# Kernel optimization log

Hardware: AMD Instinct MI355X
Metric: run time of the kernel (lower is better)

Reference implementation:

```python
import jax, jax.numpy as jnp
import numpy as np

B, L, D, H = 2, 2048, 1024, 16
HD = D // H
HID = 4 * D
EPS = 1e-5


def setup_inputs() -> dict:
    key = jax.random.key(0)
    ks = jax.random.split(key, 16)
    s = 0.02
    inp = {
        "x": jax.random.normal(ks[0], (B, L, D), jnp.float32),
        "mask": jnp.triu(jnp.ones((L, L), bool), k=1),  # True above diagonal -> masked
        "wq": jax.random.normal(ks[1], (D, D), jnp.float32) * s,
        "wk": jax.random.normal(ks[2], (D, D), jnp.float32) * s,
        "wv": jax.random.normal(ks[3], (D, D), jnp.float32) * s,
        "wo": jax.random.normal(ks[4], (D, D), jnp.float32) * s,
        "ln1_g": jnp.ones((D,), jnp.float32),
        "ln1_b": jnp.zeros((D,), jnp.float32),
        "ln2_g": jnp.ones((D,), jnp.float32),
        "ln2_b": jnp.zeros((D,), jnp.float32),
        "w1": jax.random.normal(ks[5], (HID, D), jnp.float32) * s,
        "b1": jnp.zeros((HID,), jnp.float32),
        "wg": jax.random.normal(ks[6], (HID, D), jnp.float32) * s,
        "w2": jax.random.normal(ks[7], (D, HID), jnp.float32) * s,
        "b2": jnp.zeros((D,), jnp.float32),
    }
    return inp


def _layernorm(x, g, b):
    mu = jnp.mean(x, axis=-1, keepdims=True)
    var = jnp.mean(jnp.square(x - mu), axis=-1, keepdims=True)
    return (x - mu) * jax.lax.rsqrt(var + EPS) * g + b


def _attention(h, mask, wq, wk, wv, wo):
    b, l, d = h.shape
    scale = HD ** -0.5
    # torch Linear: y = x @ W.T (W is [out, in])
    q = (h @ wq.T).reshape(b, l, H, HD)
    k = (h @ wk.T).reshape(b, l, H, HD)
    v = (h @ wv.T).reshape(b, l, H, HD)
    attn = jnp.einsum("bqhd,bkhd->bhqk", q, k) * scale
    attn = jnp.where(mask[None, None, :, :], -jnp.inf, attn)
    pos_bias = jnp.arange(l, dtype=attn.dtype) * 0.01  # additive bias along key axis
    attn = attn + pos_bias[None, None, None, :]
    attn = jax.nn.softmax(attn, axis=-1)
    out = jnp.einsum("bhqk,bkhd->bqhd", attn, v).reshape(b, l, d)
    return out @ wo.T


def _ffn(h, w1, b1, wg, w2, b2):
    return (jax.nn.silu(h @ w1.T + b1) * (h @ wg.T)) @ w2.T + b2


def reference(x, mask, wq, wk, wv, wo, ln1_g, ln1_b, ln2_g, ln2_b, w1, b1, wg, w2, b2):
    x = x + _attention(_layernorm(x, ln1_g, ln1_b), mask, wq, wk, wv, wo)
    x = x + _ffn(_layernorm(x, ln2_g, ln2_b), w1, b1, wg, w2, b2)
    return x
```

## Files before the change

kernel.cpp:

```cpp
#include <hip/hip_runtime.h>

#define ML   2048
#define MD   1024
#define MH   16
#define MHD  64
#define MB   2
#define MM   4096
#define MHID 4096

typedef unsigned short u16;
typedef short bf16x8 __attribute__((ext_vector_type(8)));
typedef float f32x4 __attribute__((ext_vector_type(4)));

__device__ __forceinline__ u16 f2bf(float f) {
    union { float f; unsigned u; } c; c.f = f;
    unsigned r = c.u + 0x7fffu + ((c.u >> 16) & 1u);
    return (u16)(r >> 16);
}
__device__ __forceinline__ float bf2f(u16 h) {
    union { unsigned u; float f; } c; c.u = ((unsigned)h) << 16;
    return c.f;
}

__device__ __forceinline__ void async_copy16(const u16* g, u16* l) {
    __builtin_amdgcn_global_load_lds(
        (const __attribute__((address_space(1))) void*)g,
        (__attribute__((address_space(3))) void*)l, 16, 0, 0);
}

struct ConvPack {
    const float* src[13];
    u16* dst[13];
    int n[13];
    int start[14];
};

__global__ __launch_bounds__(256)
void conv_all(ConvPack p)
{
    const int bx = blockIdx.x;
    int seg = 0;
    while (seg < 12 && bx >= p.start[seg + 1]) ++seg;
    const int local = bx - p.start[seg];
    const int idx = (local * 256 + threadIdx.x) * 8;
    if (idx >= p.n[seg]) return;
    const float* in = p.src[seg];
    const float4 a = *(const float4*)(in + idx);
    const float4 b = *(const float4*)(in + idx + 4);
    union { bf16x8 v; u16 s[8]; } u;
    u.s[0] = f2bf(a.x); u.s[1] = f2bf(a.y); u.s[2] = f2bf(a.z); u.s[3] = f2bf(a.w);
    u.s[4] = f2bf(b.x); u.s[5] = f2bf(b.y); u.s[6] = f2bf(b.z); u.s[7] = f2bf(b.w);
    *(bf16x8*)&p.dst[seg][idx] = u.v;
}

template<int MI, int NI>
__device__ __forceinline__ void gemm_core(
    const u16* __restrict__ A, const u16* __restrict__ Bm,
    int m0, int n0, int lda, int ldb, int K,
    u16* As, u16* Bs, f32x4 (&acc)[MI][NI])
{
    constexpr int TM = MI * 32;
    constexpr int TN = NI * 32;
    const int tid  = threadIdx.x;
    const int wave = tid >> 6, lane = tid & 63;
    const int wm = wave & 1, wn = wave >> 1;
    const int l15 = lane & 15, quad = lane >> 4;

    const int srow = wave * 16 + (lane >> 2);
    const int scol = (lane & 3) * 8;
    const u16* Ag = A  + (size_t)(m0 + srow) * lda + scol;
    const u16* Bg = Bm + (size_t)(n0 + srow) * ldb + scol;
    u16* Asw = As + srow * 32 + scol;
    u16* Bsw = Bs + srow * 32 + scol;

    f32x4 zero4 = {0.f, 0.f, 0.f, 0.f};
#pragma unroll
    for (int mi = 0; mi < MI; ++mi)
#pragma unroll
        for (int ni = 0; ni < NI; ++ni) acc[mi][ni] = zero4;

    for (int k0 = 0; k0 < K; k0 += 32) {
        __syncthreads();
#pragma unroll
        for (int p = 0; p < TM / 64; ++p)
            async_copy16(Ag + k0 + (size_t)p * 64 * lda, Asw + p * 64 * 32);
#pragma unroll
        for (int p = 0; p < TN / 64; ++p)
            async_copy16(Bg + k0 + (size_t)p * 64 * ldb, Bsw + p * 64 * 32);
        __syncthreads();

        bf16x8 af[MI], bfr[NI];
#pragma unroll
        for (int mi = 0; mi < MI; ++mi)
            af[mi] = *(const bf16x8*)&As[(wm * MI * 16 + mi * 16 + l15) * 32 + quad * 8];
#pragma unroll
        for (int ni = 0; ni < NI; ++ni)
            bfr[ni] = *(const bf16x8*)&Bs[(wn * NI * 16 + ni * 16 + l15) * 32 + quad * 8];
#pragma unroll
        for (int mi = 0; mi < MI; ++mi)
#pragma unroll
            for (int ni = 0; ni < NI; ++ni)
                acc[mi][ni] = __builtin_amdgcn_mfma_f32_16x16x32_bf16(
                    af[mi], bfr[ni], acc[mi][ni], 0, 0, 0);
    }
}

__global__ __launch_bounds__(256)
void ln_kernel(const float* __restrict__ xin,
               const u16* __restrict__ g, const u16* __restrict__ bb,
               u16* __restrict__ out,
               const u16* __restrict__ rbias, float* __restrict__ oinit)
{
    const int row = blockIdx.x;
    const int tid = threadIdx.x;
    const float4 t = *(const float4*)(xin + (size_t)row * MD + tid * 4);
    float v[4] = {t.x, t.y, t.z, t.w};
    if (oinit) {
        const ushort4 rb = *(const ushort4*)&rbias[tid * 4];
        float4 oi;
        oi.x = v[0] + bf2f(rb.x);
        oi.y = v[1] + bf2f(rb.y);
        oi.z = v[2] + bf2f(rb.z);
        oi.w = v[3] + bf2f(rb.w);
        *(float4*)&oinit[(size_t)row * MD + tid * 4] = oi;
    }
    float s  = v[0] + v[1] + v[2] + v[3];
    float s2 = v[0]*v[0] + v[1]*v[1] + v[2]*v[2] + v[3]*v[3];
#pragma unroll
    for (int off = 1; off < 64; off <<= 1) {
        s  += __shfl_xor(s,  off);
        s2 += __shfl_xor(s2, off);
    }
    __shared__ float red[8];
    const int wave = tid >> 6, lane = tid & 63;
    if (lane == 0) { red[wave] = s; red[4 + wave] = s2; }
    __syncthreads();
    s  = red[0] + red[1] + red[2] + red[3];
    s2 = red[4] + red[5] + red[6] + red[7];
    const float mu  = s * (1.0f / MD);
    const float var = fmaxf(s2 * (1.0f / MD) - mu * mu, 0.0f);
    const float rs  = rsqrtf(var + 1e-5f);
    const ushort4 gv = *(const ushort4*)&g[tid * 4];
    const ushort4 bv = *(const ushort4*)&bb[tid * 4];
    ushort4 o;
    o.x = f2bf((v[0] - mu) * rs * bf2f(gv.x) + bf2f(bv.x));
    o.y = f2bf((v[1] - mu) * rs * bf2f(gv.y) + bf2f(bv.y));
    o.z = f2bf((v[2] - mu) * rs * bf2f(gv.z) + bf2f(bv.z));
    o.w = f2bf((v[3] - mu) * rs * bf2f(gv.w) + bf2f(bv.w));
    *(ushort4*)&out[(size_t)row * MD + tid * 4] = o;
}

__global__ __launch_bounds__(256, 2)
void gemm_qkv(const u16* __restrict__ ln, const u16* __restrict__ wq,
              const u16* __restrict__ wk, const u16* __restrict__ wv,
              u16* __restrict__ q, u16* __restrict__ k, u16* __restrict__ vt)
{
    __shared__ __align__(16) u16 As[128 * 32];
    __shared__ __align__(16) u16 Bs[128 * 32];
    const int z = blockIdx.z;
    const u16* Bm = (z == 0) ? wq : (z == 1) ? wk : wv;
    const int m0 = blockIdx.x * 128, n0 = blockIdx.y * 128;
    f32x4 acc[4][4];
    gemm_core<4, 4>(ln, Bm, m0, n0, MD, MD, MD, As, Bs, acc);

    const int tid = threadIdx.x;
    const int wave = tid >> 6, lane = tid & 63;
    const int wm = wave & 1, wn = wave >> 1, l15 = lane & 15, quad = lane >> 4;
    if (z < 2) {
        u16* out = (z == 0) ? q : k;
        const float scale = (z == 0) ? 0.125f : 1.0f;
#pragma unroll
        for (int mi = 0; mi < 4; ++mi)
#pragma unroll
            for (int ni = 0; ni < 4; ++ni)
#pragma unroll
                for (int r = 0; r < 4; ++r) {
                    const int row = m0 + wm * 64 + mi * 16 + quad * 4 + r;
                    const int col = n0 + wn * 64 + ni * 16 + l15;
                    out[(size_t)row * MD + col] = f2bf(acc[mi][ni][r] * scale);
                }
    } else {
#pragma unroll
        for (int mi = 0; mi < 4; ++mi)
#pragma unroll
            for (int ni = 0; ni < 4; ++ni) {
                const int row0 = m0 + wm * 64 + mi * 16 + quad * 4;
                const int col  = n0 + wn * 64 + ni * 16 + l15;
                const int bb = row0 >> 11, l = row0 & (ML - 1);
                const int hh = col >> 6,  hd = col & (MHD - 1);
                ushort4 pk;
                pk.x = f2bf(acc[mi][ni][0]);
                pk.y = f2bf(acc[mi][ni][1]);
                pk.z = f2bf(acc[mi][ni][2]);
                pk.w = f2bf(acc[mi][ni][3]);
                *(ushort4*)&vt[((size_t)(bb * MH + hh) * MHD + hd) * ML + l] = pk;
            }
    }
}

__global__ __launch_bounds__(256, 2)
void attn_kernel(const u16* __restrict__ Q, const u16* __restrict__ Kb,
                 const u16* __restrict__ Vt, u16* __restrict__ O)
{
    __shared__ __align__(16) u16 Ks[64 * 64];
    __shared__ __align__(16) u16 Vs[64 * 64];
    __shared__ __align__(16) u16 Pl[4][16 * 72];
    const int tid = threadIdx.x, wave = tid >> 6, lane = tid & 63;
    const int quad = lane >> 4, l15 = lane & 15;
    const int idx = blockIdx.x;
    const int qt = (ML / 64 - 1) - (idx >> 5);
    const int hb = idx & 31;
    const int h = hb & 15, b = hb >> 4;
    const int q0 = qt * 64;
    const int qrow = q0 + wave * 16;
    const float L2E = 1.44269504f;
    const float C1 = 0.01f * L2E;
    const float C2 = -32.0f * L2E;

    u16* Plw = Pl[wave];

    const size_t qoff = ((size_t)(b * ML + qrow + l15)) * MD + h * MHD + quad * 8;
    const bf16x8 aq0 = *(const bf16x8*)&Q[qoff];
    const bf16x8 aq1 = *(const bf16x8*)&Q[qoff + 32];

    const int str = tid >> 3;
    const int sj  = tid & 7;
    const int sjx = (sj ^ (str & 7)) * 8;
    const u16* Kg = Kb + (size_t)(b * ML) * MD + h * MHD;
    const u16* Vg = Vt + (size_t)((b * MH + h) * MHD) * ML;

    const int rsw0 = ((quad    ) ^ (l15 & 7)) * 8;
    const int rsw1 = ((quad + 4) ^ (l15 & 7)) * 8;

    bf16x8 onesf;
    {
        const short v = (l15 == 0) ? (short)0x3F80 : (short)0;
        onesf = (bf16x8){v, v, v, v, v, v, v, v};
    }

    f32x4 zero4 = {0.f, 0.f, 0.f, 0.f};
    f32x4 Oacc[4];
    f32x4 lsum = zero4;
#pragma unroll
    for (int i = 0; i < 4; ++i) Oacc[i] = zero4;

    for (int kt = 0; kt <= qt; ++kt) {
        const int k0 = kt * 64;

        __syncthreads();
        async_copy16(Kg + (size_t)(k0 + str) * MD + sjx,        Ks + tid * 8);
        async_copy16(Kg + (size_t)(k0 + 32 + str) * MD + sjx,   Ks + 2048 + tid * 8);
        async_copy16(Vg + (size_t)str * ML + k0 + sjx,          Vs + tid * 8);
        async_copy16(Vg + (size_t)(32 + str) * ML + k0 + sjx,   Vs + 2048 + tid * 8);
        __syncthreads();

        f32x4 s[4];
#pragma unroll
        for (int jn = 0; jn < 4; ++jn) {
            const int krow = (jn * 16 + l15) * 64;
            const bf16x8 k0f = *(const bf16x8*)&Ks[krow + rsw0];
            const bf16x8 k1f = *(const bf16x8*)&Ks[krow + rsw1];
            f32x4 z = zero4;
            z = __builtin_amdgcn_mfma_f32_16x16x32_bf16(aq0, k0f, z, 0, 0, 0);
            z = __builtin_amdgcn_mfma_f32_16x16x32_bf16(aq1, k1f, z, 0, 0, 0);
            s[jn] = z;
        }

        const bool diag = (kt == qt);
#pragma unroll
        for (int jn = 0; jn < 4; ++jn) {
            const int key = k0 + jn * 16 + l15;
            const float pbm = fmaf((float)key, C1, C2);
#pragma unroll
            for (int r = 0; r < 4; ++r) {
                float val = fmaf(s[jn][r], L2E, pbm);
                if (diag && key > qrow + quad * 4 + r) val = -30000.f;
                union { float f; unsigned u; } c;
                c.f = exp2f(val);
                Plw[(quad * 4 + r) * 72 + jn * 16 + l15] = (u16)(c.u >> 16);
            }
        }

        bf16x8 vv[4][2];
#pragma unroll
        for (int j = 0; j < 4; ++j) {
            const int vrow = (j * 16 + l15) * 64;
            vv[j][0] = *(const bf16x8*)&Vs[vrow + rsw0];
            vv[j][1] = *(const bf16x8*)&Vs[vrow + rsw1];
        }

        const bf16x8 ap0 = *(const bf16x8*)&Plw[l15 * 72 + quad * 8];
        const bf16x8 ap1 = *(const bf16x8*)&Plw[l15 * 72 + 32 + quad * 8];
#pragma unroll
        for (int j = 0; j < 4; ++j) {
            Oacc[j] = __builtin_amdgcn_mfma_f32_16x16x32_bf16(ap0, vv[j][0], Oacc[j], 0, 0, 0);
            Oacc[j] = __builtin_amdgcn_mfma_f32_16x16x32_bf16(ap1, vv[j][1], Oacc[j], 0, 0, 0);
        }
        lsum = __builtin_amdgcn_mfma_f32_16x16x32_bf16(ap0, onesf, lsum, 0, 0, 0);
        lsum = __builtin_amdgcn_mfma_f32_16x16x32_bf16(ap1, onesf, lsum, 0, 0, 0);
    }

#pragma unroll
    for (int r = 0; r < 4; ++r) {
        const float l = __shfl(lsum[r], lane & 48);
        const float inv = 1.0f / l;
        const int row = qrow + quad * 4 + r;
#pragma unroll
        for (int j = 0; j < 4; ++j) {
            const int col = h * MHD + j * 16 + l15;
            O[((size_t)(b * ML + row)) * MD + col] = f2bf(Oacc[j][r] * inv);
        }
    }
}

__global__ __launch_bounds__(256, 2)
void gemm_wo(const u16* __restrict__ ao, const u16* __restrict__ wo,
             const float* __restrict__ x, float* __restrict__ h1)
{
    __shared__ __align__(16) u16 As[64 * 32];
    __shared__ __align__(16) u16 Bs[128 * 32];
    const int m0 = blockIdx.x * 64, n0 = blockIdx.y * 128;
    f32x4 acc[2][4];
    gemm_core<2, 4>(ao, wo, m0, n0, MD, MD, MD, As, Bs, acc);
    const int tid = threadIdx.x;
    const int wave = tid >> 6, lane = tid & 63;
    const int wm = wave & 1, wn = wave >> 1, l15 = lane & 15, quad = lane >> 4;
#pragma unroll
    for (int mi = 0; mi < 2; ++mi)
#pragma unroll
        for (int ni = 0; ni < 4; ++ni)
#pragma unroll
            for (int r = 0; r < 4; ++r) {
                const int row = m0 + wm * 32 + mi * 16 + quad * 4 + r;
                const int col = n0 + wn * 64 + ni * 16 + l15;
                const size_t idx = (size_t)row * MD + col;
                h1[idx] = acc[mi][ni][r] + x[idx];
            }
}

__global__ __launch_bounds__(512, 2)
void gemm_ug256(const u16* __restrict__ ln, const u16* __restrict__ w1,
                const u16* __restrict__ wg, const u16* __restrict__ b1,
                u16* __restrict__ hf)
{
    __shared__ __align__(16) u16 smem[4][16384];
    const int tid = threadIdx.x;
    const int wave = tid >> 6, lane = tid & 63;
    const int wm = wave >> 2, wn = wave & 3;
    const int l15 = lane & 15, quad = lane >> 4;
    const int m0 = blockIdx.x * 256, n0 = blockIdx.y * 128;

    const int str = tid >> 3;
    const int sjx = ((tid & 7) ^ (str & 7)) * 8;
    const u16* Ag  = ln + (size_t)(m0 + str) * MD + sjx;
    const u16* B1g = w1 + (size_t)(n0 + str) * MD + sjx;
    const u16* B2g = wg + (size_t)(n0 + str) * MD + sjx;

    f32x4 zero4 = {0.f, 0.f, 0.f, 0.f};
    f32x4 acc[8][4];
#pragma unroll
    for (int mi = 0; mi < 8; ++mi)
#pragma unroll
        for (int ni = 0; ni < 4; ++ni) acc[mi][ni] = zero4;

#define UG_STAGE(d, k0)                                                        \
    do {                                                                       \
        _Pragma("unroll")                                                      \
        for (int p = 0; p < 4; ++p)                                            \
            async_copy16(Ag + (size_t)p * 64 * MD + (k0),                      \
                         &smem[d][p * 4096 + tid * 8]);                        \
        _Pragma("unroll")                                                      \
        for (int p = 0; p < 2; ++p)                                            \
            async_copy16(B1g + (size_t)p * 64 * MD + (k0),                     \
                         &smem[2 + (d)][p * 4096 + tid * 8]);                  \
        _Pragma("unroll")                                                      \
        for (int p = 0; p < 2; ++p)                                            \
            async_copy16(B2g + (size_t)p * 64 * MD + (k0),                     \
                         &smem[2 + (d)][(p + 2) * 4096 + tid * 8]);            \
    } while (0)

    UG_STAGE(0, 0);

    for (int t = 0; t < 16; ++t) {
        const int d = t & 1;
        const u16* Abuf = smem[d];
        const u16* Bbuf = smem[2 + d];

        if (t < 15) {
            UG_STAGE(d ^ 1, (t + 1) * 64);
            asm volatile("s_waitcnt vmcnt(8)" ::: "memory");
        } else {
            asm volatile("s_waitcnt vmcnt(0)" ::: "memory");
        }
        __builtin_amdgcn_s_barrier();
        __builtin_amdgcn_sched_barrier(0);

        bf16x8 bfr[4][2], af0[4][2];
#pragma unroll
        for (int ni = 0; ni < 4; ++ni)
#pragma unroll
            for (int kh = 0; kh < 2; ++kh)
                bfr[ni][kh] = *(const bf16x8*)&Bbuf[(wn * 64 + ni * 16 + l15) * 64
                                                    + ((kh * 4 + quad) ^ (l15 & 7)) * 8];
#pragma unroll
        for (int mi = 0; mi < 4; ++mi)
#pragma unroll
            for (int kh = 0; kh < 2; ++kh)
                af0[mi][kh] = *(const bf16x8*)&Abuf[(wm * 128 + mi * 16 + l15) * 64
                                                    + ((kh * 4 + quad) ^ (l15 & 7)) * 8];

        __builtin_amdgcn_s_setprio(1);
#pragma unroll
        for (int mi = 0; mi < 4; ++mi)
#pragma unroll
            for (int ni = 0; ni < 4; ++ni) {
                acc[mi][ni] = __builtin_amdgcn_mfma_f32_16x16x32_bf16(
                    af0[mi][0], bfr[ni][0], acc[mi][ni], 0, 0, 0);
                acc[mi][ni] = __builtin_amdgcn_mfma_f32_16x16x32_bf16(
                    af0[mi][1], bfr[ni][1], acc[mi][ni], 0, 0, 0);
            }
        __builtin_amdgcn_s_setprio(0);
        __builtin_amdgcn_s_barrier();

        bf16x8 af1[4][2];
#pragma unroll
        for (int mi = 0; mi < 4; ++mi)
#pragma unroll
            for (int kh = 0; kh < 2; ++kh)
                af1[mi][kh] = *(const bf16x8*)&Abuf[(wm * 128 + (mi + 4) * 16 + l15) * 64
                                                    + ((kh * 4 + quad) ^ (l15 & 7)) * 8];
        __builtin_amdgcn_s_setprio(1);
#pragma unroll
        for (int mi = 0; mi < 4; ++mi)
#pragma unroll
            for (int ni = 0; ni < 4; ++ni) {
                acc[mi + 4][ni] = __builtin_amdgcn_mfma_f32_16x16x32_bf16(
                    af1[mi][0], bfr[ni][0], acc[mi + 4][ni], 0, 0, 0);
                acc[mi + 4][ni] = __builtin_amdgcn_mfma_f32_16x16x32_bf16(
                    af1[mi][1], bfr[ni][1], acc[mi + 4][ni], 0, 0, 0);
            }
        __builtin_amdgcn_s_setprio(0);

        __builtin_amdgcn_s_barrier();
        __builtin_amdgcn_sched_barrier(0);
    }
#undef UG_STAGE

    float* X = (float*)&smem[0][0];
    if (wn < 2) {
        float* Xw = X + (wm * 2 + wn) * 8192;
#pragma unroll
        for (int mi = 0; mi < 8; ++mi)
#pragma unroll
            for (int ni = 0; ni < 4; ++ni)
#pragma unroll
                for (int r = 0; r < 4; ++r)
                    Xw[((mi * 4 + ni) * 4 + r) * 64 + lane] = acc[mi][ni][r];
    }
    __syncthreads();
    if (wn >= 2) {
        const float* Xw = X + (wm * 2 + (wn - 2)) * 8192;
#pragma unroll
        for (int mi = 0; mi < 8; ++mi)
#pragma unroll
            for (int ni = 0; ni < 4; ++ni) {
                const int col = n0 + (wn - 2) * 64 + ni * 16 + l15;
                const float bb1 = bf2f(b1[col]);
#pragma unroll
                for (int r = 0; r < 4; ++r) {
                    const int row = m0 + wm * 128 + mi * 16 + quad * 4 + r;
                    const float uv = Xw[((mi * 4 + ni) * 4 + r) * 64 + lane] + bb1;
                    const float si = uv / (1.0f + __expf(-uv));
                    hf[(size_t)row * MHID + col] = f2bf(si * acc[mi][ni][r]);
                }
            }
    }
}

__global__ __launch_bounds__(256, 2)
void gemm_w2(const u16* __restrict__ hf, const u16* __restrict__ w2,
             float* __restrict__ out)
{
    __shared__ __align__(16) u16 As[128 * 32];
    __shared__ __align__(16) u16 Bs[128 * 32];
    const int m0 = blockIdx.x * 128, n0 = blockIdx.y * 128;
    const int kz = blockIdx.z * 2048;
    f32x4 acc[4][4];
    gemm_core<4, 4>(hf + kz, w2 + kz, m0, n0, MHID, MHID, 2048, As, Bs, acc);
    const int tid = threadIdx.x;
    const int wave = tid >> 6, lane = tid & 63;
    const int wm = wave & 1, wn = wave >> 1, l15 = lane & 15, quad = lane >> 4;
#pragma unroll
    for (int mi = 0; mi < 4; ++mi)
#pragma unroll
        for (int ni = 0; ni < 4; ++ni)
#pragma unroll
            for (int r = 0; r < 4; ++r) {
                const int row = m0 + wm * 64 + mi * 16 + quad * 4 + r;
                const int col = n0 + wn * 64 + ni * 16 + l15;
                unsafeAtomicAdd(&out[(size_t)row * MD + col], acc[mi][ni][r]);
            }
}

extern "C" void kernel_launch(void* const* d_in, const int* in_sizes, int n_in,
                              void* d_out, int out_size, void* d_ws, size_t ws_size,
                              hipStream_t stream)
{
    const float* x    = (const float*)d_in[0];
    const float* wq   = (const float*)d_in[2];
    const float* wk   = (const float*)d_in[3];
    const float* wv   = (const float*)d_in[4];
    const float* wo   = (const float*)d_in[5];
    const float* ln1g = (const float*)d_in[6];
    const float* ln1b = (const float*)d_in[7];
    const float* ln2g = (const float*)d_in[8];
    const float* ln2b = (const float*)d_in[9];
    const float* w1   = (const float*)d_in[10];
    const float* b1   = (const float*)d_in[11];
    const float* wgp  = (const float*)d_in[12];
    const float* w2   = (const float*)d_in[13];
    const float* b2   = (const float*)d_in[14];
    float* out = (float*)d_out;

    char* ws = (char*)d_ws;
    u16*  wqb  = (u16*)(ws);
    u16*  wkb  = (u16*)(ws + ((size_t)2  << 20));
    u16*  wvb  = (u16*)(ws + ((size_t)4  << 20));
    u16*  wob  = (u16*)(ws + ((size_t)6  << 20));
    u16*  w1b  = (u16*)(ws + ((size_t)8  << 20));
    u16*  wgb  = (u16*)(ws + ((size_t)16 << 20));
    u16*  w2b  = (u16*)(ws + ((size_t)24 << 20));
    char* vec  = ws + ((size_t)32 << 20);
    u16*  l1g  = (u16*)(vec);
    u16*  l1b  = (u16*)(vec + 4096);
    u16*  l2g  = (u16*)(vec + 8192);
    u16*  l2b  = (u16*)(vec + 12288);
    u16*  b1b  = (u16*)(vec + 16384);
    u16*  b2b  = (u16*)(vec + 24576);
    u16*   ln  = (u16*)(ws + ((size_t)33 << 20));
    u16*   q   = (u16*)(ws + ((size_t)41 << 20));
    u16*   k   = (u16*)(ws + ((size_t)49 << 20));
    u16*   vt  = (u16*)(ws + ((size_t)57 << 20));
    u16*   ao  = ln;
    float* h1  = (float*)(ws + ((size_t)41 << 20));
    u16*   hf  = (u16*)(ws + ((size_t)89 << 20));

    const int NW = MD * MD;
    const int NF = MHID * MD;
    ConvPack cp;
    const float* srcs[13] = {wq, wk, wv, wo, w1, wgp, w2, ln1g, ln1b, ln2g, ln2b, b1, b2};
    u16* dsts[13]         = {wqb, wkb, wvb, wob, w1b, wgb, w2b, l1g, l1b, l2g, l2b, b1b, b2b};
    int  ns[13]           = {NW, NW, NW, NW, NF, NF, NF, MD, MD, MD, MD, MHID, MD};
    int start = 0;
    for (int i = 0; i < 13; ++i) {
        cp.src[i] = srcs[i]; cp.dst[i] = dsts[i]; cp.n[i] = ns[i];
        cp.start[i] = start;
        start += (ns[i] + 2047) / 2048;
    }
    cp.start[13] = start;
    conv_all<<<start, 256, 0, stream>>>(cp);

    ln_kernel<<<MM, 256, 0, stream>>>(x, l1g, l1b, ln, nullptr, nullptr);
    gemm_qkv<<<dim3(MM / 128, MD / 128, 3), 256, 0, stream>>>(ln, wqb, wkb, wvb, q, k, vt);
    attn_kernel<<<(ML / 64) * MH * MB, 256, 0, stream>>>(q, k, vt, ao);
    gemm_wo<<<dim3(MM / 64, MD / 128), 256, 0, stream>>>(ao, wob, x, h1);
    ln_kernel<<<MM, 256, 0, stream>>>(h1, l2g, l2b, ln, b2b, out);
    gemm_ug256<<<dim3(MM / 256, MHID / 128), 512, 0, stream>>>(ln, w1b, wgb, b1b, hf);
    gemm_w2<<<dim3(MM / 128, MD / 128, 2), 256, 0, stream>>>(hf, w2b, out);
}
```

Measured before the change: 400.9 us.

## Split up/gate GEMM k-step into four phases and stagger B prefetch

```diff
diff --git a/kernel.cpp b/kernel.cpp
--- a/kernel.cpp
+++ b/kernel.cpp
@@ -363,12 +363,15 @@
 #pragma unroll
         for (int ni = 0; ni < 4; ++ni) acc[mi][ni] = zero4;
 
-#define UG_STAGE(d, k0)                                                        \
+#define UG_STAGE_A(d, k0)                                                      \
     do {                                                                       \
         _Pragma("unroll")                                                      \
         for (int p = 0; p < 4; ++p)                                            \
             async_copy16(Ag + (size_t)p * 64 * MD + (k0),                      \
                          &smem[d][p * 4096 + tid * 8]);                        \
+    } while (0)
+#define UG_STAGE_B(d, k0)                                                      \
+    do {                                                                       \
         _Pragma("unroll")                                                      \
         for (int p = 0; p < 2; ++p)                                            \
             async_copy16(B1g + (size_t)p * 64 * MD + (k0),                     \
@@ -379,7 +382,12 @@
                          &smem[2 + (d)][(p + 2) * 4096 + tid * 8]);            \
     } while (0)
 
-    UG_STAGE(0, 0);
+    UG_STAGE_A(0, 0);
+    UG_STAGE_B(0, 0);
+
+    const int Arow = wm * 128;
+    const int Brow = wn * 64;
+    const int swz  = (l15 & 7);
 
     for (int t = 0; t < 16; ++t) {
         const int d = t & 1;
@@ -387,64 +395,84 @@
         const u16* Bbuf = smem[2 + d];
 
         if (t < 15) {
-            UG_STAGE(d ^ 1, (t + 1) * 64);
-            asm volatile("s_waitcnt vmcnt(8)" ::: "memory");
+            UG_STAGE_A(d ^ 1, (t + 1) * 64);
+            asm volatile("s_waitcnt vmcnt(4)" ::: "memory");
         } else {
             asm volatile("s_waitcnt vmcnt(0)" ::: "memory");
         }
         __builtin_amdgcn_s_barrier();
-        __builtin_amdgcn_sched_barrier(0);
-
-        bf16x8 bfr[4][2], af0[4][2];
+
+        bf16x8 b0[4], a0[4];
 #pragma unroll
         for (int ni = 0; ni < 4; ++ni)
-#pragma unroll
-            for (int kh = 0; kh < 2; ++kh)
-                bfr[ni][kh] = *(const bf16x8*)&Bbuf[(wn * 64 + ni * 16 + l15) * 64
-                                                    + ((kh * 4 + quad) ^ (l15 & 7)) * 8];
-#pragma unroll
-        for (int mi = 0; mi < 4; ++mi)
-#pragma unroll
-            for (int kh = 0; kh < 2; ++kh)
-                af0[mi][kh] = *(const bf16x8*)&Abuf[(wm * 128 + mi * 16 + l15) * 64
-                                                    + ((kh * 4 + quad) ^ (l15 & 7)) * 8];
-
+            b0[ni] = *(const bf16x8*)&Bbuf[(Brow + ni * 16 + l15) * 64
+                                            + (quad ^ swz) * 8];
+#pragma unroll
+        for (int mi = 0; mi < 4; ++mi)
+            a0[mi] = *(const bf16x8*)&Abuf[(Arow + mi * 16 + l15) * 64
+                                            + (quad ^ swz) * 8];
         __builtin_amdgcn_s_setprio(1);
 #pragma unroll
         for (int mi = 0; mi < 4; ++mi)
 #pragma unroll
-            for (int ni = 0; ni < 4; ++ni) {
+            for (int ni = 0; ni < 4; ++ni)
                 acc[mi][ni] = __builtin_amdgcn_mfma_f32_16x16x32_bf16(
-                    af0[mi][0], bfr[ni][0], acc[mi][ni], 0, 0, 0);
-                acc[mi][ni] = __builtin_amdgcn_mfma_f32_16x16x32_bf16(
-                    af0[mi][1], bfr[ni][1], acc[mi][ni], 0, 0, 0);
-            }
+                    a0[mi], b0[ni], acc[mi][ni], 0, 0, 0);
         __builtin_amdgcn_s_setprio(0);
         __builtin_amdgcn_s_barrier();
 
-        bf16x8 af1[4][2];
-#pragma unroll
-        for (int mi = 0; mi < 4; ++mi)
-#pragma unroll
-            for (int kh = 0; kh < 2; ++kh)
-                af1[mi][kh] = *(const bf16x8*)&Abuf[(wm * 128 + (mi + 4) * 16 + l15) * 64
-                                                    + ((kh * 4 + quad) ^ (l15 & 7)) * 8];
+        if (t < 15) UG_STAGE_B(d ^ 1, (t + 1) * 64);
+        bf16x8 a1[4];
+#pragma unroll
+        for (int mi = 0; mi < 4; ++mi)
+            a1[mi] = *(const bf16x8*)&Abuf[(Arow + (mi + 4) * 16 + l15) * 64
+                                            + (quad ^ swz) * 8];
         __builtin_amdgcn_s_setprio(1);
 #pragma unroll
         for (int mi = 0; mi < 4; ++mi)
 #pragma unroll
-            for (int ni = 0; ni < 4; ++ni) {
+            for (int ni = 0; ni < 4; ++ni)
                 acc[mi + 4][ni] = __builtin_amdgcn_mfma_f32_16x16x32_bf16(
-                    af1[mi][0], bfr[ni][0], acc[mi + 4][ni], 0, 0, 0);
+                    a1[mi], b0[ni], acc[mi + 4][ni], 0, 0, 0);
+        __builtin_amdgcn_s_setprio(0);
+        __builtin_amdgcn_s_barrier();
+
+        bf16x8 bh[4], a2[4];
+#pragma unroll
+        for (int ni = 0; ni < 4; ++ni)
+            bh[ni] = *(const bf16x8*)&Bbuf[(Brow + ni * 16 + l15) * 64
+                                            + ((4 + quad) ^ swz) * 8];
+#pragma unroll
+        for (int mi = 0; mi < 4; ++mi)
+            a2[mi] = *(const bf16x8*)&Abuf[(Arow + mi * 16 + l15) * 64
+                                            + ((4 + quad) ^ swz) * 8];
+        __builtin_amdgcn_s_setprio(1);
+#pragma unroll
+        for (int mi = 0; mi < 4; ++mi)
+#pragma unroll
+            for (int ni = 0; ni < 4; ++ni)
+                acc[mi][ni] = __builtin_amdgcn_mfma_f32_16x16x32_bf16(
+                    a2[mi], bh[ni], acc[mi][ni], 0, 0, 0);
+        __builtin_amdgcn_s_setprio(0);
+        __builtin_amdgcn_s_barrier();
+
+        bf16x8 a3[4];
+#pragma unroll
+        for (int mi = 0; mi < 4; ++mi)
+            a3[mi] = *(const bf16x8*)&Abuf[(Arow + (mi + 4) * 16 + l15) * 64
+                                            + ((4 + quad) ^ swz) * 8];
+        __builtin_amdgcn_s_setprio(1);
+#pragma unroll
+        for (int mi = 0; mi < 4; ++mi)
+#pragma unroll
+            for (int ni = 0; ni < 4; ++ni)
                 acc[mi + 4][ni] = __builtin_amdgcn_mfma_f32_16x16x32_bf16(
-                    af1[mi][1], bfr[ni][1], acc[mi + 4][ni], 0, 0, 0);
-            }
+                    a3[mi], bh[ni], acc[mi + 4][ni], 0, 0, 0);
         __builtin_amdgcn_s_setprio(0);
-
         __builtin_amdgcn_s_barrier();
-        __builtin_amdgcn_sched_barrier(0);
-    }
-#undef UG_STAGE
+    }
+#undef UG_STAGE_A
+#undef UG_STAGE_B
 
     float* X = (float*)&smem[0][0];
     if (wn < 2) {
```

Result: no change. 399.5 us (-0.4%).
